# Kernel optimization log

Hardware: AMD Instinct MI355X
Metric: run time of the kernel (lower is better)

## Reference

```python
import jax, jax.numpy as jnp
import numpy as np


def setup_inputs() -> dict:
    key = jax.random.key(0)
    k1, k2 = jax.random.split(key)
    B, S, D_IN, D_OUT = 4, 8192, 768, 768
    x = jax.random.normal(k1, (B, S, D_IN), dtype=jnp.float32)
    # kaiming_normal_(mode='fan_out', nonlinearity='linear') -> std = 1/sqrt(fan_out)
    weight = jax.random.normal(k2, (D_OUT, D_IN), dtype=jnp.float32) * (1.0 / jnp.sqrt(D_OUT))
    return {"x": x, "weight": weight}


def reference(x, weight):
    # Binarize weights with sign (0 -> 0, matching torch.sign), then F.linear:
    # out[..., o] = sum_i x[..., i] * sign(W)[o, i]
    w_bin = jnp.sign(weight)
    return jnp.einsum('bsi,oi->bso', x, w_bin)
```

## Files before the change

### kernel.cpp

```cpp
#include <hip/hip_runtime.h>
#include <hip/hip_bf16.h>

using f32x4 = __attribute__((ext_vector_type(4))) float;
using s16x8 = __attribute__((ext_vector_type(8))) short;

constexpr int KDIM = 768;
constexpr int NDIM = 768;
constexpr int BM = 128;
constexpr int BN = 128;
constexpr int BK = 32;
constexpr int NBN = NDIM / BN;
constexpr int NT = KDIM / BK;

__device__ __forceinline__ unsigned short f2bf(float f) {
    __bf16 h = (__bf16)f;
    return __builtin_bit_cast(unsigned short, h);
}

__device__ __forceinline__ short sgnbf(float w) {
    unsigned u = __builtin_bit_cast(unsigned, w);
    return (w != 0.f) ? (short)(unsigned short)(0x3F80u | ((u >> 16) & 0x8000u))
                      : (short)0;
}

__device__ __forceinline__ s16x8 cvt8(float4 u, float4 v) {
    s16x8 c;
    c[0] = (short)f2bf(u.x); c[1] = (short)f2bf(u.y);
    c[2] = (short)f2bf(u.z); c[3] = (short)f2bf(u.w);
    c[4] = (short)f2bf(v.x); c[5] = (short)f2bf(v.y);
    c[6] = (short)f2bf(v.z); c[7] = (short)f2bf(v.w);
    return c;
}

__global__ void binarize_w(const float* __restrict__ W, unsigned short* __restrict__ Wf) {
    const int g = blockIdx.x * 256 + threadIdx.x;
    const int lane = g & 63;
    const int grp  = g >> 6;
    const int n16l = grp & 7;
    const int bkt  = grp >> 3;
    const int bn   = bkt % NBN;
    const int kt   = bkt / NBN;
    const int col  = bn * 128 + n16l * 16 + (lane & 15);
    const int k0   = kt * 32 + (lane >> 4) * 8;
    const float* src = W + (size_t)col * KDIM + k0;
    s16x8 r;
    #pragma unroll
    for (int j = 0; j < 8; ++j) r[j] = sgnbf(src[j]);
    *(s16x8*)(Wf + (size_t)g * 8) = r;
}

#define BAR_NODRAIN() do {                                        \
    asm volatile("s_waitcnt lgkmcnt(0)" ::: "memory");            \
    __builtin_amdgcn_s_barrier();                                 \
    asm volatile("" ::: "memory");                                \
} while (0)

template<bool PRE>
__global__ __launch_bounds__(256, 4)
void binlin_mfma(const float* __restrict__ X, const float* __restrict__ W,
                 const unsigned short* __restrict__ Wf, float* __restrict__ Out) {
    __shared__ __align__(16) unsigned short As[2][512 * 8];
    __shared__ __align__(16) unsigned short Bs[2][512 * 8];

    const int bid = blockIdx.x;
    const int cpx = gridDim.x >> 3;
    const int swz = (bid & 7) * cpx + (bid >> 3);
    const int bm = swz / NBN;
    const int bn = swz - bm * NBN;

    const int t    = threadIdx.x;
    const int lane = t & 63;
    const int wid  = t >> 6;
    const int wm   = (wid >> 1) * 64;
    const int wn   = (wid & 1) * 64;
    const int wm16 = (wid >> 1) * 4;
    const int wn16 = (wid & 1) * 4;

    const float* Xb = X + (size_t)bm * BM * KDIM;

    const int r   = t >> 2;
    const int c8  = (t & 3) * 8;
    const float* Abase = Xb + (size_t)r * KDIM + c8;
    const int sA1 = (r >> 4) * 64 + (r & 15) + 16 * (t & 3);
    const int sA2 = sA1 + 256;

    float4 aR[4];
    s16x8  bR[2];

    auto loadA = [&](int kt) {
        const float* p = Abase + kt * BK;
        aR[0] = *(const float4*)p;
        aR[1] = *(const float4*)(p + 4);
        aR[2] = *(const float4*)(p + (size_t)64 * KDIM);
        aR[3] = *(const float4*)(p + (size_t)64 * KDIM + 4);
    };
    auto writeA = [&](int buf) {
        *(s16x8*)&As[buf][(size_t)sA1 * 8] = cvt8(aR[0], aR[1]);
        *(s16x8*)&As[buf][(size_t)sA2 * 8] = cvt8(aR[2], aR[3]);
    };
    auto loadB = [&](int kt) {
        if constexpr (PRE) {
            const unsigned short* q = Wf + ((size_t)(kt * NBN + bn) * 512 + 2 * t) * 8;
            bR[0] = *(const s16x8*)q;
            bR[1] = *(const s16x8*)(q + 8);
        } else {
            #pragma unroll
            for (int i = 0; i < 2; ++i) {
                const int s    = 2 * t + i;
                const int col  = bn * 128 + (s >> 6) * 16 + (s & 15);
                const int k0   = kt * 32 + ((s >> 4) & 3) * 8;
                const float* wp = W + (size_t)col * KDIM + k0;
                float4 u = *(const float4*)wp;
                float4 v = *(const float4*)(wp + 4);
                s16x8 c;
                c[0] = sgnbf(u.x); c[1] = sgnbf(u.y); c[2] = sgnbf(u.z); c[3] = sgnbf(u.w);
                c[4] = sgnbf(v.x); c[5] = sgnbf(v.y); c[6] = sgnbf(v.z); c[7] = sgnbf(v.w);
                bR[i] = c;
            }
        }
    };
    auto writeB = [&](int buf) {
        *(s16x8*)&Bs[buf][(size_t)(2 * t) * 8]     = bR[0];
        *(s16x8*)&Bs[buf][(size_t)(2 * t + 1) * 8] = bR[1];
    };

    f32x4 acc[4][4] = {};

    loadA(0); loadB(0);
    writeA(0); writeB(0);
    BAR_NODRAIN();

    #pragma unroll 2
    for (int kt = 0; kt < NT; ++kt) {
        const int c = kt & 1;
        const bool pf = (kt + 1 < NT);

        if (pf) { loadA(kt + 1); loadB(kt + 1); }

        s16x8 af[4], bf_[4];
        #pragma unroll
        for (int m = 0; m < 4; ++m)
            af[m] = *(const s16x8*)&As[c][(size_t)((wm16 + m) * 64 + lane) * 8];
        #pragma unroll
        for (int n = 0; n < 4; ++n)
            bf_[n] = *(const s16x8*)&Bs[c][(size_t)((wn16 + n) * 64 + lane) * 8];

        #pragma unroll
        for (int m = 0; m < 4; ++m)
            #pragma unroll
            for (int n = 0; n < 4; ++n)
                acc[m][n] = __builtin_amdgcn_mfma_f32_16x16x32_bf16(
                    af[m], bf_[n], acc[m][n], 0, 0, 0);

        if (pf) {
            writeA(c ^ 1); writeB(c ^ 1);
            BAR_NODRAIN();
        }
    }

    float* Ob = Out + (size_t)(bm * BM) * NDIM + bn * BN;
    const int lr = lane & 15;
    #pragma unroll
    for (int m = 0; m < 4; ++m) {
        const int row0 = wm + m * 16 + (lane >> 4) * 4;
        #pragma unroll
        for (int n = 0; n < 4; ++n) {
            const int col = wn + n * 16 + lr;
            #pragma unroll
            for (int rr = 0; rr < 4; ++rr)
                Ob[(size_t)(row0 + rr) * NDIM + col] = acc[m][n][rr];
        }
    }
}

extern "C" void kernel_launch(void* const* d_in, const int* in_sizes, int n_in,
                              void* d_out, int out_size, void* d_ws, size_t ws_size,
                              hipStream_t stream) {
    const float* X = (const float*)d_in[0];
    const float* W = (const float*)d_in[1];
    float* Out = (float*)d_out;
    const int M = in_sizes[0] / KDIM;
    const int grid = (M / BM) * NBN;
    const size_t need = (size_t)NDIM * KDIM * sizeof(unsigned short);

    if (ws_size >= need) {
        unsigned short* Wf = (unsigned short*)d_ws;
        binarize_w<<<(NT * NBN * 8 * 64) / 256, 256, 0, stream>>>(W, Wf);
        binlin_mfma<true><<<grid, 256, 0, stream>>>(X, W, Wf, Out);
    } else {
        binlin_mfma<false><<<grid, 256, 0, stream>>>(X, W, nullptr, Out);
    }
}
```

Before: 60.73 us.

## Deepen register prefetch to two K-tiles ahead and fully unroll main loop

Global loads for A and B are now issued two K-iterations ahead using two alternating register sets, so each load has a full extra MFMA iteration to land before it is converted and stored to LDS. The K loop is fully unrolled so the ping-pong register selection resolves at compile time, and launch bounds drop from 4 to 3 waves per SIMD to leave room for the extra registers. The aim is to hide global memory latency better. The cost is higher register pressure, lower occupancy and larger code size.

After: 60.91 us. Within noise of the previous version (+0.3%).

```diff
diff --git a/kernel.cpp b/kernel.cpp
--- a/kernel.cpp
+++ b/kernel.cpp
@@ -56,7 +56,7 @@
 } while (0)
 
 template<bool PRE>
-__global__ __launch_bounds__(256, 4)
+__global__ __launch_bounds__(256, 3)
 void binlin_mfma(const float* __restrict__ X, const float* __restrict__ W,
                  const unsigned short* __restrict__ Wf, float* __restrict__ Out) {
     __shared__ __align__(16) unsigned short As[2][512 * 8];
@@ -84,25 +84,22 @@
     const int sA1 = (r >> 4) * 64 + (r & 15) + 16 * (t & 3);
     const int sA2 = sA1 + 256;
 
-    float4 aR[4];
-    s16x8  bR[2];
-
-    auto loadA = [&](int kt) {
+    auto loadA = [&](int kt, float4 a[4]) {
         const float* p = Abase + kt * BK;
-        aR[0] = *(const float4*)p;
-        aR[1] = *(const float4*)(p + 4);
-        aR[2] = *(const float4*)(p + (size_t)64 * KDIM);
-        aR[3] = *(const float4*)(p + (size_t)64 * KDIM + 4);
+        a[0] = *(const float4*)p;
+        a[1] = *(const float4*)(p + 4);
+        a[2] = *(const float4*)(p + (size_t)64 * KDIM);
+        a[3] = *(const float4*)(p + (size_t)64 * KDIM + 4);
     };
-    auto writeA = [&](int buf) {
-        *(s16x8*)&As[buf][(size_t)sA1 * 8] = cvt8(aR[0], aR[1]);
-        *(s16x8*)&As[buf][(size_t)sA2 * 8] = cvt8(aR[2], aR[3]);
+    auto writeA = [&](int buf, float4 a[4]) {
+        *(s16x8*)&As[buf][(size_t)sA1 * 8] = cvt8(a[0], a[1]);
+        *(s16x8*)&As[buf][(size_t)sA2 * 8] = cvt8(a[2], a[3]);
     };
-    auto loadB = [&](int kt) {
+    auto loadB = [&](int kt, s16x8 b[2]) {
         if constexpr (PRE) {
             const unsigned short* q = Wf + ((size_t)(kt * NBN + bn) * 512 + 2 * t) * 8;
-            bR[0] = *(const s16x8*)q;
-            bR[1] = *(const s16x8*)(q + 8);
+            b[0] = *(const s16x8*)q;
+            b[1] = *(const s16x8*)(q + 8);
         } else {
             #pragma unroll
             for (int i = 0; i < 2; ++i) {
@@ -115,27 +112,33 @@
                 s16x8 c;
                 c[0] = sgnbf(u.x); c[1] = sgnbf(u.y); c[2] = sgnbf(u.z); c[3] = sgnbf(u.w);
                 c[4] = sgnbf(v.x); c[5] = sgnbf(v.y); c[6] = sgnbf(v.z); c[7] = sgnbf(v.w);
-                bR[i] = c;
+                b[i] = c;
             }
         }
     };
-    auto writeB = [&](int buf) {
-        *(s16x8*)&Bs[buf][(size_t)(2 * t) * 8]     = bR[0];
-        *(s16x8*)&Bs[buf][(size_t)(2 * t + 1) * 8] = bR[1];
+    auto writeB = [&](int buf, s16x8 b[2]) {
+        *(s16x8*)&Bs[buf][(size_t)(2 * t) * 8]     = b[0];
+        *(s16x8*)&Bs[buf][(size_t)(2 * t + 1) * 8] = b[1];
     };
 
     f32x4 acc[4][4] = {};
+    float4 A0[4], A1[4];
+    s16x8  B0[2], B1[2];
 
-    loadA(0); loadB(0);
-    writeA(0); writeB(0);
+    loadA(0, A0); loadB(0, B0);
+    loadA(1, A1); loadB(1, B1);
+    writeA(0, A0); writeB(0, B0);
     BAR_NODRAIN();
 
-    #pragma unroll 2
+    #pragma unroll
     for (int kt = 0; kt < NT; ++kt) {
         const int c = kt & 1;
-        const bool pf = (kt + 1 < NT);
+        float4 (&AFree)[4] = c ? A1 : A0;
+        float4 (&AWr)[4]   = c ? A0 : A1;
+        s16x8  (&BFree)[2] = c ? B1 : B0;
+        s16x8  (&BWr)[2]   = c ? B0 : B1;
 
-        if (pf) { loadA(kt + 1); loadB(kt + 1); }
+        if (kt + 2 < NT) { loadA(kt + 2, AFree); loadB(kt + 2, BFree); }
 
         s16x8 af[4], bf_[4];
         #pragma unroll
@@ -152,8 +155,8 @@
                 acc[m][n] = __builtin_amdgcn_mfma_f32_16x16x32_bf16(
                     af[m], bf_[n], acc[m][n], 0, 0, 0);
 
-        if (pf) {
-            writeA(c ^ 1); writeB(c ^ 1);
+        if (kt + 1 < NT) {
+            writeA(c ^ 1, AWr); writeB(c ^ 1, BWr);
             BAR_NODRAIN();
         }
     }
```

## Halve M tile, stage binarized weights via global_load_lds DMA, raise occupancy

Applied to the files above, without the earlier changes.

Cuts the block M tile from 128 to 64 rows, so each wave now holds a 32x64 output tile and register and LDS use drop. Occupancy target goes from 4 to 6 blocks per SM. The pre-binarized weight tile is now copied straight from global memory into LDS with global_load_lds, skipping the register round trip. The custom no-drain barrier is replaced by __syncthreads, which adds a full vmcnt drain, and weight reuse per block is halved, so global traffic for weights rises.

Result: slower. 67.96 us (+11.9%).

```diff
diff --git a/kernel.cpp b/kernel.cpp
--- a/kernel.cpp
+++ b/kernel.cpp
@@ -6,7 +6,7 @@
 
 constexpr int KDIM = 768;
 constexpr int NDIM = 768;
-constexpr int BM = 128;
+constexpr int BM = 64;
 constexpr int BN = 128;
 constexpr int BK = 32;
 constexpr int NBN = NDIM / BN;
@@ -49,17 +49,18 @@
     *(s16x8*)(Wf + (size_t)g * 8) = r;
 }
 
-#define BAR_NODRAIN() do {                                        \
-    asm volatile("s_waitcnt lgkmcnt(0)" ::: "memory");            \
-    __builtin_amdgcn_s_barrier();                                 \
-    asm volatile("" ::: "memory");                                \
-} while (0)
+__device__ __forceinline__ void gload_lds16(const void* g, void* l) {
+    __builtin_amdgcn_global_load_lds(
+        (const __attribute__((address_space(1))) unsigned int*)g,
+        (__attribute__((address_space(3))) unsigned int*)l,
+        16, 0, 0);
+}
 
 template<bool PRE>
-__global__ __launch_bounds__(256, 4)
+__global__ __launch_bounds__(256, 6)
 void binlin_mfma(const float* __restrict__ X, const float* __restrict__ W,
                  const unsigned short* __restrict__ Wf, float* __restrict__ Out) {
-    __shared__ __align__(16) unsigned short As[2][512 * 8];
+    __shared__ __align__(16) unsigned short As[2][256 * 8];
     __shared__ __align__(16) unsigned short Bs[2][512 * 8];
 
     const int bid = blockIdx.x;
@@ -71,101 +72,97 @@
     const int t    = threadIdx.x;
     const int lane = t & 63;
     const int wid  = t >> 6;
-    const int wm   = (wid >> 1) * 64;
-    const int wn   = (wid & 1) * 64;
-    const int wm16 = (wid >> 1) * 4;
-    const int wn16 = (wid & 1) * 4;
+    const int wr   = wid >> 1;
+    const int wc   = wid & 1;
+    const int wm16 = wr * 2;
+    const int wn16 = wc * 4;
 
-    const float* Xb = X + (size_t)bm * BM * KDIM;
+    const int r = t >> 2;
+    const int q = t & 3;
+    const float* Abase = X + (size_t)(bm * BM + r) * KDIM + q * 8;
+    const int sA = (r >> 4) * 64 + (r & 15) + 16 * q;
 
-    const int r   = t >> 2;
-    const int c8  = (t & 3) * 8;
-    const float* Abase = Xb + (size_t)r * KDIM + c8;
-    const int sA1 = (r >> 4) * 64 + (r & 15) + 16 * (t & 3);
-    const int sA2 = sA1 + 256;
-
-    float4 aR[4];
-    s16x8  bR[2];
-
+    float4 aR[2];
     auto loadA = [&](int kt) {
         const float* p = Abase + kt * BK;
         aR[0] = *(const float4*)p;
         aR[1] = *(const float4*)(p + 4);
-        aR[2] = *(const float4*)(p + (size_t)64 * KDIM);
-        aR[3] = *(const float4*)(p + (size_t)64 * KDIM + 4);
     };
     auto writeA = [&](int buf) {
-        *(s16x8*)&As[buf][(size_t)sA1 * 8] = cvt8(aR[0], aR[1]);
-        *(s16x8*)&As[buf][(size_t)sA2 * 8] = cvt8(aR[2], aR[3]);
+        *(s16x8*)&As[buf][(size_t)sA * 8] = cvt8(aR[0], aR[1]);
     };
-    auto loadB = [&](int kt) {
-        if constexpr (PRE) {
-            const unsigned short* q = Wf + ((size_t)(kt * NBN + bn) * 512 + 2 * t) * 8;
-            bR[0] = *(const s16x8*)q;
-            bR[1] = *(const s16x8*)(q + 8);
-        } else {
-            #pragma unroll
-            for (int i = 0; i < 2; ++i) {
-                const int s    = 2 * t + i;
-                const int col  = bn * 128 + (s >> 6) * 16 + (s & 15);
-                const int k0   = kt * 32 + ((s >> 4) & 3) * 8;
-                const float* wp = W + (size_t)col * KDIM + k0;
-                float4 u = *(const float4*)wp;
-                float4 v = *(const float4*)(wp + 4);
-                s16x8 c;
-                c[0] = sgnbf(u.x); c[1] = sgnbf(u.y); c[2] = sgnbf(u.z); c[3] = sgnbf(u.w);
-                c[4] = sgnbf(v.x); c[5] = sgnbf(v.y); c[6] = sgnbf(v.z); c[7] = sgnbf(v.w);
-                bR[i] = c;
-            }
+    auto stageB_dma = [&](int buf, int kt) {
+        const unsigned short* chunk = Wf + (size_t)(kt * NBN + bn) * 512 * 8;
+        #pragma unroll
+        for (int i = 0; i < 2; ++i) {
+            const int slotbase = (i * 4 + wid) * 64;
+            gload_lds16(chunk + (size_t)(slotbase + lane) * 8,
+                        &Bs[buf][(size_t)slotbase * 8]);
         }
     };
-    auto writeB = [&](int buf) {
-        *(s16x8*)&Bs[buf][(size_t)(2 * t) * 8]     = bR[0];
-        *(s16x8*)&Bs[buf][(size_t)(2 * t + 1) * 8] = bR[1];
+    auto stageB_reg = [&](int buf, int kt) {
+        #pragma unroll
+        for (int i = 0; i < 2; ++i) {
+            const int s   = t + i * 256;
+            const int col = bn * 128 + (s >> 6) * 16 + (s & 15);
+            const int k0  = kt * 32 + ((s >> 4) & 3) * 8;
+            const float* wp = W + (size_t)col * KDIM + k0;
+            float4 u = *(const float4*)wp;
+            float4 v = *(const float4*)(wp + 4);
+            s16x8 c;
+            c[0] = sgnbf(u.x); c[1] = sgnbf(u.y); c[2] = sgnbf(u.z); c[3] = sgnbf(u.w);
+            c[4] = sgnbf(v.x); c[5] = sgnbf(v.y); c[6] = sgnbf(v.z); c[7] = sgnbf(v.w);
+            *(s16x8*)&Bs[buf][(size_t)s * 8] = c;
+        }
     };
 
-    f32x4 acc[4][4] = {};
+    f32x4 acc[2][4] = {};
 
-    loadA(0); loadB(0);
-    writeA(0); writeB(0);
-    BAR_NODRAIN();
+    loadA(0);
+    writeA(0);
+    if constexpr (PRE) stageB_dma(0, 0); else stageB_reg(0, 0);
+    __syncthreads();
 
     #pragma unroll 2
     for (int kt = 0; kt < NT; ++kt) {
         const int c = kt & 1;
         const bool pf = (kt + 1 < NT);
 
-        if (pf) { loadA(kt + 1); loadB(kt + 1); }
+        if (pf) {
+            if constexpr (PRE) stageB_dma(c ^ 1, kt + 1);
+            loadA(kt + 1);
+        }
 
-        s16x8 af[4], bf_[4];
+        s16x8 af[2], bf_[4];
         #pragma unroll
-        for (int m = 0; m < 4; ++m)
+        for (int m = 0; m < 2; ++m)
             af[m] = *(const s16x8*)&As[c][(size_t)((wm16 + m) * 64 + lane) * 8];
         #pragma unroll
         for (int n = 0; n < 4; ++n)
             bf_[n] = *(const s16x8*)&Bs[c][(size_t)((wn16 + n) * 64 + lane) * 8];
 
         #pragma unroll
-        for (int m = 0; m < 4; ++m)
+        for (int m = 0; m < 2; ++m)
             #pragma unroll
             for (int n = 0; n < 4; ++n)
                 acc[m][n] = __builtin_amdgcn_mfma_f32_16x16x32_bf16(
                     af[m], bf_[n], acc[m][n], 0, 0, 0);
 
         if (pf) {
-            writeA(c ^ 1); writeB(c ^ 1);
-            BAR_NODRAIN();
+            writeA(c ^ 1);
+            if constexpr (!PRE) stageB_reg(c ^ 1, kt + 1);
         }
+        __syncthreads();
     }
 
-    float* Ob = Out + (size_t)(bm * BM) * NDIM + bn * BN;
+    float* Ob = Out + (size_t)(bm * BM + wr * 32) * NDIM + bn * BN + wc * 64;
     const int lr = lane & 15;
     #pragma unroll
-    for (int m = 0; m < 4; ++m) {
-        const int row0 = wm + m * 16 + (lane >> 4) * 4;
+    for (int m = 0; m < 2; ++m) {
+        const int row0 = m * 16 + (lane >> 4) * 4;
         #pragma unroll
         for (int n = 0; n < 4; ++n) {
-            const int col = wn + n * 16 + lr;
+            const int col = n * 16 + lr;
             #pragma unroll
             for (int rr = 0; rr < 4; ++rr)
                 Ob[(size_t)(row0 + rr) * NDIM + col] = acc[m][n][rr];
```
